# Kernel tuning notes

Hardware: AMD Instinct MI355X
Metric: run time of the kernel (lower is better)

## Reference

```python
import jax, jax.numpy as jnp
import numpy as np

B, T, DIM = 4, 1024, 2048
N_HEADS, N_KV_HEADS = 32, 8
HEAD_DIM = DIM // N_HEADS  # 64
N_REPS = N_HEADS // N_KV_HEADS  # 4


def setup_inputs() -> dict:
    key = jax.random.key(0)
    ks = jax.random.split(key, 8)
    # RoPE tables: theta = 10000^{-2i/d}, positions 0..T-1
    inv_freq = 1.0 / (10000.0 ** (jnp.arange(0, HEAD_DIM, 2, dtype=jnp.float32) / HEAD_DIM))
    angles = jnp.arange(T, dtype=jnp.float32)[:, None] * inv_freq[None, :]  # (T, HEAD_DIM//2)
    s = 0.02
    return {
        "input": jax.random.normal(ks[0], (B, T, DIM), jnp.float32),
        "freqs_cos": jnp.cos(angles),
        "freqs_sin": jnp.sin(angles),
        "mask": jnp.tril(jnp.ones((T, T), dtype=bool)),  # causal boolean mask
        "wq": s * jax.random.normal(ks[1], (DIM, DIM), jnp.float32),
        "wk": s * jax.random.normal(ks[2], (N_KV_HEADS * HEAD_DIM, DIM), jnp.float32),
        "wv": s * jax.random.normal(ks[3], (N_KV_HEADS * HEAD_DIM, DIM), jnp.float32),
        "wo": s * jax.random.normal(ks[4], (DIM, DIM), jnp.float32),
        "curr_pos": 0,
    }


def _apply_rope(x, cos, sin):
    # x: (B, T, H, D); cos/sin: (T, D//2). Complex multiply on (even, odd) pairs.
    xr = x[..., 0::2]
    xi = x[..., 1::2]
    c = cos[None, :, None, :]
    s = sin[None, :, None, :]
    out_r = xr * c - xi * s
    out_i = xr * s + xi * c
    return jnp.stack([out_r, out_i], axis=-1).reshape(x.shape)


def reference(input, freqs_cos, freqs_sin, mask, wq, wk, wv, wo, curr_pos):
    Bv, Tv = input.shape[0], input.shape[1]
    qs = (input @ wq.T).reshape(Bv, Tv, N_HEADS, HEAD_DIM)
    ks = (input @ wk.T).reshape(Bv, Tv, N_KV_HEADS, HEAD_DIM)
    vs = (input @ wv.T).reshape(Bv, Tv, N_KV_HEADS, HEAD_DIM)
    qs = _apply_rope(qs, freqs_cos, freqs_sin)
    ks = _apply_rope(ks, freqs_cos, freqs_sin)

    # KV cache (prefill path: curr_pos == 0, fresh cache of length 2T)
    kv_cache = jnp.zeros((Bv, 2 * Tv, N_KV_HEADS, HEAD_DIM, 2), input.dtype)
    kv_cache = kv_cache.at[:, curr_pos:curr_pos + Tv, :, :, 0].set(ks)
    kv_cache = kv_cache.at[:, curr_pos:curr_pos + Tv, :, :, 1].set(vs)
    k_all = kv_cache[:, :curr_pos + Tv, :, :, 0]
    v_all = kv_cache[:, :curr_pos + Tv, :, :, 1]

    # GQA: broadcast each kv head across its query-head group (avoid repeat_interleave copy)
    S = k_all.shape[1]
    q = qs.transpose(0, 2, 1, 3).reshape(Bv, N_KV_HEADS, N_REPS, Tv, HEAD_DIM)
    k = k_all.transpose(0, 2, 1, 3)  # (B, KVH, S, D)
    v = v_all.transpose(0, 2, 1, 3)

    scale = 1.0 / jnp.sqrt(jnp.asarray(HEAD_DIM, input.dtype))
    scores = jnp.einsum("bgrqd,bgkd->bgrqk", q, k) * scale  # (B, KVH, REPS, T, S)
    neg = jnp.asarray(jnp.finfo(input.dtype).min, input.dtype)
    scores = jnp.where(mask[None, None, None, :, :S], scores, neg)
    attn = jax.nn.softmax(scores, axis=-1)
    out = jnp.einsum("bgrqk,bgkd->bgrqd", attn, v)
    out = out.reshape(Bv, N_HEADS, Tv, HEAD_DIM).transpose(0, 2, 1, 3).reshape(Bv, Tv, DIM)
    return out @ wo.T
```

## Files before the change

### kernel.cpp

```cpp
#include <hip/hip_runtime.h>
#include <cstdint>

typedef __bf16 bf16x8 __attribute__((ext_vector_type(8)));
typedef float  f32x4  __attribute__((ext_vector_type(4)));
typedef float  f32x16 __attribute__((ext_vector_type(16)));
typedef float  float8v __attribute__((ext_vector_type(8)));
typedef unsigned short ushort8v __attribute__((ext_vector_type(8)));
typedef unsigned short ushort4v __attribute__((ext_vector_type(4)));
typedef unsigned int   uint4v   __attribute__((ext_vector_type(4)));

__device__ __forceinline__ unsigned short f2b(float f) {
  uint32_t u = __builtin_bit_cast(uint32_t, f);
  u += 0x7FFFu + ((u >> 16) & 1u);
  return (unsigned short)(u >> 16);
}
__device__ __forceinline__ float b2f(unsigned short h) {
  uint32_t u = ((uint32_t)h) << 16;
  return __builtin_bit_cast(float, u);
}
__device__ __forceinline__ unsigned int cvtpk(float lo, float hi_) {
  unsigned int r;
  asm("v_cvt_pk_bf16_f32 %0, %1, %2" : "=v"(r) : "v"(lo), "v"(hi_));
  return r;
}

__device__ __forceinline__ void async16(const void* g, void* l) {
  __builtin_amdgcn_global_load_lds(
      (const __attribute__((address_space(1))) void*)g,
      (__attribute__((address_space(3))) void*)l, 16, 0, 0);
}

#define WAITVM(N)  __builtin_amdgcn_s_waitcnt(0x0F70 | ((N) & 15))

struct CvtArgs {
  const float* src[5];
  unsigned short* dst[5];
  long n[5];
};
__global__ void cvt5_kernel(CvtArgs a) {
  long base = (long)blockIdx.x * blockDim.x + threadIdx.x;
  long gstride = (long)gridDim.x * blockDim.x;
#pragma unroll 1
  for (int sg = 0; sg < 5; ++sg) {
    const float* s = a.src[sg];
    unsigned short* d = a.dst[sg];
    long n8 = a.n[sg] >> 3;
    for (long i = base; i < n8; i += gstride) {
      float8v f = *(const float8v*)(s + i * 8);
      ushort8v o;
#pragma unroll
      for (int j = 0; j < 8; ++j) o[j] = f2b(f[j]);
      *(ushort8v*)(d + i * 8) = o;
    }
  }
}

__global__ __launch_bounds__(512, 2)
void gemmQ192(const unsigned short* __restrict__ Ag, const unsigned short* __restrict__ Wg,
              unsigned short* __restrict__ Cp) {
  constexpr int K = 2048;
  constexpr int NF = 3;
  constexpr int ASLOT = 16384;
  constexpr int BSLOT = 24576;
  constexpr int N = 3072;

  extern __shared__ char lds_c[];

  const int tid = threadIdx.x;
  const int wave = tid >> 6, lane = tid & 63;
  const int wm = wave >> 2, wn = wave & 3;
  const int lr = lane & 15, lg = lane >> 4;

  const int flat = blockIdx.y * 16 + blockIdx.x;
  const int swz = (flat & 7) * 32 + (flat >> 3);
  const int m0 = (swz >> 4) * 256, n0 = (swz & 15) * 192;

  const int laneSw = (lr >> 1) * 128 + (((((lr & 1) << 2) | lg) ^ (lr >> 1)) << 4);
  const int aoff = wm * 8192 + laneSw;

  int bByte[NF], bR7[NF];
#pragma unroll
  for (int ni = 0; ni < NF; ++ni) {
    int row = wn * 48 + ni * 16 + lr;
    bByte[ni] = row * 128;
    bR7[ni] = row & 7;
  }

  f32x4 acc[8][NF] = {};
  bf16x8 af[4], bf[NF];

  auto stA = [&](int slot, int s) {
    char* sl = lds_c + slot * ASLOT;
    const int kc = s * 32;
#pragma unroll
    for (int j = 0; j < 2; ++j) {
      int q = (tid + 512 * j) * 16;
      int R = q >> 7, g2L = ((q >> 4) & 7) ^ (R & 7);
      int row = R * 2 + (g2L >> 2), kg = g2L & 3;
      async16(Ag + (size_t)(m0 + row) * K + kc + kg * 8, sl + q);
    }
  };
  auto stB = [&](int slot, int T) {
    char* sl = lds_c + 4 * ASLOT + slot * BSLOT;
    const int kc = T * 64;
#pragma unroll
    for (int j = 0; j < 3; ++j) {
      int q = (tid + 512 * j) * 16;
      int row = q >> 7, c = (q >> 4) & 7;
      async16(Wg + (size_t)(n0 + row) * K + kc + ((c ^ (row & 7)) * 8), sl + q);
    }
  };

#define PH(SA, SB, MH, KH, RDB, STG, VM)                                      \
  {                                                                           \
    const char* As_ = lds_c + (SA) * ASLOT;                                   \
    _Pragma("unroll") for (int mi = 0; mi < 4; ++mi)                          \
      af[mi] = *(const bf16x8*)(As_ + aoff + ((MH) * 4 + mi) * 1024);         \
    if (RDB) {                                                                \
      const char* Bs_ = lds_c + 4 * ASLOT + (SB) * BSLOT;                     \
      _Pragma("unroll") for (int ni = 0; ni < NF; ++ni)                       \
        bf[ni] = *(const bf16x8*)(Bs_ + bByte[ni] +                           \
                                  (((((KH) << 2) | lg) ^ bR7[ni]) << 4));     \
    }                                                                         \
    STG;                                                                      \
    if ((VM) >= 0) WAITVM(VM);                                                \
    __builtin_amdgcn_s_barrier();                                             \
    __builtin_amdgcn_s_setprio(1);                                            \
    _Pragma("unroll") for (int mi = 0; mi < 4; ++mi)                          \
      _Pragma("unroll") for (int ni = 0; ni < NF; ++ni)                       \
        acc[(MH) * 4 + mi][ni] = __builtin_amdgcn_mfma_f32_16x16x32_bf16(     \
            af[mi], bf[ni], acc[(MH) * 4 + mi][ni], 0, 0, 0);                 \
    __builtin_amdgcn_s_setprio(0);                                            \
    __builtin_amdgcn_s_barrier();                                             \
  }

  stB(0, 0); stA(0, 0); stA(1, 1); stB(1, 1); stA(2, 2);
  WAITVM(5);
  __builtin_amdgcn_s_barrier();

  for (int t2 = 0; t2 < 30; t2 += 2) {
    PH(0, 0, 0, 0, true,  stA(3, 2 * t2 + 3), -1);
    PH(0, 0, 1, 0, false, (void)0, -1);
    PH(1, 0, 0, 1, true,  stA(0, 2 * t2 + 4), -1);
    PH(1, 0, 1, 1, false, stB(0, t2 + 2), 5);
    PH(2, 1, 0, 0, true,  stA(1, 2 * t2 + 5), -1);
    PH(2, 1, 1, 0, false, (void)0, -1);
    PH(3, 1, 0, 1, true,  stA(2, 2 * t2 + 6), -1);
    PH(3, 1, 1, 1, false, stB(1, t2 + 3), 5);
  }
  PH(0, 0, 0, 0, true,  stA(3, 63), -1);
  PH(0, 0, 1, 0, false, (void)0, -1);
  PH(1, 0, 0, 1, true,  (void)0, -1);
  PH(1, 0, 1, 1, false, (void)0, 0);
  PH(2, 1, 0, 0, true,  (void)0, -1);
  PH(2, 1, 1, 0, false, (void)0, -1);
  PH(3, 1, 0, 1, true,  (void)0, -1);
  PH(3, 1, 1, 1, false, (void)0, -1);
#undef PH

#pragma unroll
  for (int mig = 0; mig < 8; ++mig) {
#pragma unroll
    for (int j = 0; j < 4; ++j) {
      int row = m0 + wm * 128 + mig * 16 + lg * 4 + j;
#pragma unroll
      for (int ni = 0; ni < NF; ++ni) {
        int col = n0 + wn * 48 + ni * 16 + lr;
        Cp[(size_t)row * N + col] = f2b(acc[mig][ni][j]);
      }
    }
  }
}

template<bool F32OUT, int BN, int GX, int GY>
__global__ __launch_bounds__(512, 2)
void gemm8p(const unsigned short* __restrict__ Ag, const unsigned short* __restrict__ Wg,
            void* __restrict__ Cp, int N) {
  constexpr int K = 2048;
  constexpr int BM = 256;
  constexpr int NF = BN / 64;
  constexpr int AL = 2;
  constexpr int BL = BN / 128;
  constexpr int VMS = 2 * BL + AL;
  constexpr int ASLOT = BM * 64;
  constexpr int BSLOT = BN * 64;
  constexpr int NWG = GX * GY;
  constexpr int CPX = NWG / 8;

  extern __shared__ char lds_c[];

  const int tid = threadIdx.x;
  const int wave = tid >> 6, lane = tid & 63;
  const int wm = wave >> 2, wn = wave & 3;
  const int lr = lane & 15, lg = lane >> 4;

  const int flat = blockIdx.y * GX + blockIdx.x;
  const int swz = (flat & 7) * CPX + (flat >> 3);
  const int m0 = (swz / GX) * BM, n0 = (swz % GX) * BN;

  const int laneSw = (lr >> 1) * 128 + (((((lr & 1) << 2) | lg) ^ (lr >> 1)) << 4);
  const int aoff = wm * 128 * 64 + laneSw;
  const int boff = wn * NF * 1024 + laneSw;

  f32x4 acc[8][NF] = {};
  bf16x8 af[4], bf[NF];

  auto stA = [&](int slot, int s) {
    char* sl = lds_c + slot * ASLOT;
    const int kc = s * 32;
#pragma unroll
    for (int j = 0; j < AL; ++j) {
      int q = (tid + 512 * j) * 16;
      int R = q >> 7, g2L = ((q >> 4) & 7) ^ (R & 7);
      int row = R * 2 + (g2L >> 2), kg = g2L & 3;
      async16(Ag + (size_t)(m0 + row) * K + kc + kg * 8, sl + q);
    }
  };
  auto stB = [&](int slot, int s) {
    char* sl = lds_c + 4 * ASLOT + slot * BSLOT;
    const int kc = s * 32;
#pragma unroll
    for (int j = 0; j < BL; ++j) {
      int q = (tid + 512 * j) * 16;
      int R = q >> 7, g2L = ((q >> 4) & 7) ^ (R & 7);
      int row = R * 2 + (g2L >> 2), kg = g2L & 3;
      async16(Wg + (size_t)(n0 + row) * K + kc + kg * 8, sl + q);
    }
  };

#define PH(RSLOT, MH, RDB, STG, VM)                                           \
  {                                                                           \
    const char* As_ = lds_c + (RSLOT) * ASLOT;                                \
    _Pragma("unroll") for (int mi = 0; mi < 4; ++mi)                          \
      af[mi] = *(const bf16x8*)(As_ + aoff + ((MH) * 4 + mi) * 1024);         \
    if (RDB) {                                                                \
      const char* Bs_ = lds_c + 4 * ASLOT + (RSLOT) * BSLOT;                  \
      _Pragma("unroll") for (int ni = 0; ni < NF; ++ni)                       \
        bf[ni] = *(const bf16x8*)(Bs_ + boff + ni * 1024);                    \
    }                                                                         \
    STG;                                                                      \
    if ((VM) >= 0) WAITVM(VM);                                                \
    __builtin_amdgcn_s_barrier();                                             \
    __builtin_amdgcn_s_setprio(1);                                            \
    _Pragma("unroll") for (int mi = 0; mi < 4; ++mi)                          \
      _Pragma("unroll") for (int ni = 0; ni < NF; ++ni)                       \
        acc[(MH) * 4 + mi][ni] = __builtin_amdgcn_mfma_f32_16x16x32_bf16(     \
            af[mi], bf[ni], acc[(MH) * 4 + mi][ni], 0, 0, 0);                 \
    __builtin_amdgcn_s_setprio(0);                                            \
    __builtin_amdgcn_s_barrier();                                             \
  }

  stB(0, 0); stA(0, 0); stB(1, 1); stA(1, 1); stB(2, 2); stA(2, 2); stB(3, 3);
  WAITVM(VMS);
  __builtin_amdgcn_s_barrier();

  for (int T = 0; T < 30; T += 2) {
    const int p0 = 2 * T;
    PH(0, 0, true,  stA(3, p0 + 3), -1);
    PH(0, 1, false, stB(0, p0 + 4), -1);
    PH(1, 0, true,  stA(0, p0 + 4), -1);
    PH(1, 1, false, stB(1, p0 + 5), VMS);
    PH(2, 0, true,  stA(1, p0 + 5), -1);
    PH(2, 1, false, stB(2, p0 + 6), -1);
    PH(3, 0, true,  stA(2, p0 + 6), -1);
    PH(3, 1, false, stB(3, p0 + 7), VMS);
  }
  PH(0, 0, true,  stA(3, 63), -1);
  PH(0, 1, false, (void)0, -1);
  PH(1, 0, true,  (void)0, -1);
  PH(1, 1, false, (void)0, 0);
  PH(2, 0, true,  (void)0, -1);
  PH(2, 1, false, (void)0, -1);
  PH(3, 0, true,  (void)0, -1);
  PH(3, 1, false, (void)0, -1);
#undef PH

#pragma unroll
  for (int mig = 0; mig < 8; ++mig) {
#pragma unroll
    for (int j = 0; j < 4; ++j) {
      int row = m0 + wm * 128 + mig * 16 + lg * 4 + j;
#pragma unroll
      for (int ni = 0; ni < NF; ++ni) {
        int col = n0 + wn * (NF * 16) + ni * 16 + lr;
        float v = acc[mig][ni][j];
        if (F32OUT) ((float*)Cp)[(size_t)row * N + col] = v;
        else        ((unsigned short*)Cp)[(size_t)row * N + col] = f2b(v);
      }
    }
  }
}

__global__ __launch_bounds__(256)
void ropekv_kernel(unsigned short* __restrict__ qkv,
                   const float* __restrict__ cosb, const float* __restrict__ sinb,
                   unsigned short* __restrict__ vt) {
  const int tt0 = blockIdx.x * 64;
  const int kvh = blockIdx.y;
  const int b   = blockIdx.z;
  const int tid = threadIdx.x;

  {
    int r = tid >> 2, c0 = (tid & 3) * 16;
    int t = tt0 + r;
    unsigned short* kp = qkv + (size_t)(b * 1024 + t) * 3072 + 2048 + kvh * 64 + c0;
    const float* cb = cosb + t * 32 + c0 / 2;
    const float* sb = sinb + t * 32 + c0 / 2;
    ushort8v x0 = *(const ushort8v*)kp;
    ushort8v x1 = *(const ushort8v*)(kp + 8);
    float8v c = *(const float8v*)cb;
    float8v s = *(const float8v*)sb;
    ushort8v o0, o1;
#pragma unroll
    for (int j = 0; j < 4; ++j) {
      float xr = b2f(x0[2 * j]), xi = b2f(x0[2 * j + 1]);
      o0[2 * j]     = f2b(xr * c[j] - xi * s[j]);
      o0[2 * j + 1] = f2b(xr * s[j] + xi * c[j]);
    }
#pragma unroll
    for (int j = 0; j < 4; ++j) {
      float xr = b2f(x1[2 * j]), xi = b2f(x1[2 * j + 1]);
      o1[2 * j]     = f2b(xr * c[4 + j] - xi * s[4 + j]);
      o1[2 * j + 1] = f2b(xr * s[4 + j] + xi * c[4 + j]);
    }
    *(ushort8v*)kp = o0;
    *(ushort8v*)(kp + 8) = o1;
  }

  __shared__ unsigned short lT[64 * 68];
#pragma unroll
  for (int i = 0; i < 2; ++i) {
    int r = i * 32 + (tid >> 3), c = (tid & 7) * 8;
    const unsigned short* src = qkv + (size_t)(b * 1024 + tt0 + r) * 3072 + 2560 + kvh * 64 + c;
    ushort8v v = *(const ushort8v*)src;
    ushort4v a, b4;
#pragma unroll
    for (int j = 0; j < 4; ++j) { a[j] = v[j]; b4[j] = v[j + 4]; }
    *(ushort4v*)&lT[r * 68 + c]     = a;
    *(ushort4v*)&lT[r * 68 + c + 4] = b4;
  }
  __syncthreads();
#pragma unroll
  for (int i = 0; i < 2; ++i) {
    int d = tid & 63;
    int tt = i * 4 + (tid >> 6);
    ushort8v o;
#pragma unroll
    for (int j = 0; j < 8; ++j) o[j] = lT[(tt * 8 + j) * 68 + d];
    *(ushort8v*)&vt[((size_t)((b * 8 + kvh) * 64 + d)) * 1024 + tt0 + tt * 8] = o;
  }
}

__global__ __launch_bounds__(256, 2)
void attn_kernel(const unsigned short* __restrict__ qkv, const unsigned short* __restrict__ vt,
                 const float* __restrict__ cosb, const float* __restrict__ sinb,
                 unsigned short* __restrict__ ob) {
  const int flat = (blockIdx.z * 8 + blockIdx.y) * 16 + blockIdx.x;
  const int swzb = (flat & 7) * 64 + (flat >> 3);
  const int bx = swzb & 15, kvh = (swzb >> 4) & 7, b = swzb >> 7;

  const int tid = threadIdx.x, wave = tid >> 6, lane = tid & 63;
  const int l31 = lane & 31, hi = lane >> 5;
  const int h = kvh * 4 + wave;

  const int qth = 31 - bx, qtl = bx;
  const int q0h = qth * 32, q0l = qtl * 32;
  const int nth = qth / 4 + 1, ntl = qtl / 4 + 1;
  const int ntot = nth + ntl;

  __shared__ unsigned short lK[2][128 * 64];
  __shared__ unsigned short lVt[2][64 * 128];

  auto ldq = [&](int q0, bf16x8* qf) {
    int t = q0 + l31;
    const unsigned short* qp = qkv + (size_t)(b * 1024 + t) * 3072 + h * 64;
#pragma unroll
    for (int dk = 0; dk < 4; ++dk) {
      ushort8v q = *(const ushort8v*)(qp + dk * 16 + hi * 8);
      f32x4 c4 = *(const f32x4*)(cosb + t * 32 + dk * 8 + hi * 4);
      f32x4 s4 = *(const f32x4*)(sinb + t * 32 + dk * 8 + hi * 4);
      ushort8v o;
#pragma unroll
      for (int j = 0; j < 4; ++j) {
        float xr = b2f(q[2 * j]), xi = b2f(q[2 * j + 1]);
        o[2 * j]     = f2b(xr * c4[j] - xi * s4[j]);
        o[2 * j + 1] = f2b(xr * s4[j] + xi * c4[j]);
      }
      qf[dk] = __builtin_bit_cast(bf16x8, o);
    }
  };

  const unsigned short* kg = qkv + (size_t)(b * 1024) * 3072 + 2048 + kvh * 64;
  const unsigned short* vg = vt + (size_t)(b * 8 + kvh) * 64 * 1024;

  auto stage = [&](int kvb, int bi) {
    const int sr  = tid >> 3;
    const int scb = (tid & 7) * 16;
#pragma unroll
    for (int i = 0; i < 4; ++i) {
      int r = i * 32 + sr;
      int cb = scb ^ ((r & 7) << 4);
      async16(kg + (size_t)(kvb + r) * 3072 + (cb >> 1), &lK[bi][r * 64 + (scb >> 1)]);
    }
    const int rv0 = tid >> 4;
    const int scv = (tid & 15) * 16;
#pragma unroll
    for (int i = 0; i < 4; ++i) {
      int rv = i * 16 + rv0;
      int cbv = scv ^ ((rv & 15) << 4);
      async16(vg + (size_t)rv * 1024 + kvb + (cbv >> 1), &lVt[bi][rv * 128 + (scv >> 1)]);
    }
  };

  bf16x8 qf[4];
  f32x16 oacc[2] = {};
  float m2 = -3e38f, l_run = 0.f;
  int q0 = q0h;

  ldq(q0h, qf);

  const float SC = 0.125f * 1.44269504f;

  auto chunk64 = [&](int cur, int ckvb, int c, bool lastT) {
    f32x16 sd[2] = {};
    __builtin_amdgcn_s_setprio(1);
#pragma unroll
    for (int s = 0; s < 2; ++s) {
      const int krow = c * 64 + s * 32 + l31;
      const char* kr = (const char*)lK[cur] + krow * 128;
      const int swz = (krow & 7) << 4;
#pragma unroll
      for (int dk = 0; dk < 4; ++dk) {
        bf16x8 kf = *(const bf16x8*)(kr + ((dk * 32 + hi * 16) ^ swz));
        sd[s] = __builtin_amdgcn_mfma_f32_32x32x16_bf16(kf, qf[dk], sd[s], 0, 0, 0);
      }
    }
    __builtin_amdgcn_s_setprio(0);

#pragma unroll
    for (int s = 0; s < 2; ++s)
#pragma unroll
      for (int r = 0; r < 16; ++r) {
        float v = sd[s][r] * SC;
        if (lastT) {
          int kvg = ckvb + s * 32 + (r & 3) + 8 * (r >> 2) + 4 * hi;
          if (kvg > q0 + l31) v = -3e38f;
        }
        sd[s][r] = v;
      }
    float pm = sd[0][0];
#pragma unroll
    for (int s = 0; s < 2; ++s)
#pragma unroll
      for (int r = 0; r < 16; ++r) pm = fmaxf(pm, sd[s][r]);
    pm = fmaxf(pm, __shfl_xor(pm, 32));
    if (!__all(pm <= m2 + 11.0f)) {
      float mnew = fmaxf(m2, pm);
      float alpha = exp2f(m2 - mnew);
      m2 = mnew;
      l_run *= alpha;
#pragma unroll
      for (int db = 0; db < 2; ++db)
#pragma unroll
        for (int r = 0; r < 16; ++r) oacc[db][r] *= alpha;
    }
    float tsum = 0.f;
#pragma unroll
    for (int s = 0; s < 2; ++s)
#pragma unroll
      for (int r = 0; r < 16; ++r) { float p = exp2f(sd[s][r] - m2); sd[s][r] = p; tsum += p; }
    tsum += __shfl_xor(tsum, 32);
    l_run += tsum;

    bf16x8 pf[2][2];
#pragma unroll
    for (int s = 0; s < 2; ++s)
#pragma unroll
      for (int kc = 0; kc < 2; ++kc) {
        unsigned int cA = cvtpk(sd[s][8 * kc + 0], sd[s][8 * kc + 1]);
        unsigned int cB = cvtpk(sd[s][8 * kc + 4], sd[s][8 * kc + 5]);
        unsigned int cC = cvtpk(sd[s][8 * kc + 2], sd[s][8 * kc + 3]);
        unsigned int cD = cvtpk(sd[s][8 * kc + 6], sd[s][8 * kc + 7]);
        unsigned int xA = __shfl_xor(cA, 32), xB = __shfl_xor(cB, 32);
        unsigned int xC = __shfl_xor(cC, 32), xD = __shfl_xor(cD, 32);
        uint4v u;
        u[0] = hi ? xB : cA;
        u[1] = hi ? xD : cC;
        u[2] = hi ? cB : xA;
        u[3] = hi ? cD : xC;
        pf[s][kc] = __builtin_bit_cast(bf16x8, u);
      }

    __builtin_amdgcn_s_setprio(1);
#pragma unroll
    for (int db = 0; db < 2; ++db) {
      const int row = db * 32 + l31;
      const char* vr = (const char*)lVt[cur] + row * 256;
      const int vswz = (row & 15) << 4;
#pragma unroll
      for (int s = 0; s < 2; ++s)
#pragma unroll
        for (int kc = 0; kc < 2; ++kc) {
          bf16x8 vf = *(const bf16x8*)(vr + ((c * 128 + s * 64 + kc * 32 + hi * 16) ^ vswz));
          oacc[db] = __builtin_amdgcn_mfma_f32_32x32x16_bf16(vf, pf[s][kc], oacc[db], 0, 0, 0);
        }
    }
    __builtin_amdgcn_s_setprio(0);
  };

  auto writeOut = [&](int q0w) {
    float inv = 1.0f / l_run;
    unsigned short* orow = ob + (size_t)(b * 1024 + q0w + l31) * 2048 + h * 64;
#pragma unroll
    for (int db = 0; db < 2; ++db)
#pragma unroll
      for (int g = 0; g < 4; ++g) {
        int d0 = db * 32 + 8 * g + 4 * hi;
        ushort4v o;
#pragma unroll
        for (int j = 0; j < 4; ++j) o[j] = f2b(oacc[db][4 * g + j] * inv);
        *(ushort4v*)(orow + d0) = o;
      }
  };

  auto kvb_of = [&](int j) { return (j < nth ? j : j - nth) * 128; };

  stage(0, 0);
  __syncthreads();

  for (int j = 0; j < ntot; ++j) {
    const int cur = j & 1;
    if (j + 1 < ntot) stage(kvb_of(j + 1), cur ^ 1);
    const int kvb = kvb_of(j);
    const bool lastT = (j == nth - 1) || (j == ntot - 1);

#pragma unroll 1
    for (int c = 0; c < 2; ++c) {
      if (kvb + c * 64 > q0 + 31) continue;
      chunk64(cur, kvb + c * 64, c, lastT);
    }

    if (j == nth - 1) {
      writeOut(q0h);
      oacc[0] = f32x16{}; oacc[1] = f32x16{};
      m2 = -3e38f; l_run = 0.f;
      q0 = q0l;
      ldq(q0l, qf);
    }
    __syncthreads();
  }
  writeOut(q0l);
}

extern "C" void kernel_launch(void* const* d_in, const int* in_sizes, int n_in,
                              void* d_out, int out_size, void* d_ws, size_t ws_size,
                              hipStream_t stream) {
  const float* input = (const float*)d_in[0];
  const float* fcos  = (const float*)d_in[1];
  const float* fsin  = (const float*)d_in[2];
  const float* wq = (const float*)d_in[4];
  const float* wk = (const float*)d_in[5];
  const float* wv = (const float*)d_in[6];
  const float* wo = (const float*)d_in[7];
  float* out = (float*)d_out;

  unsigned short* xb   = (unsigned short*)d_ws;
  unsigned short* wqkv = xb + (size_t)4096 * 2048;
  unsigned short* wob  = wqkv + (size_t)3072 * 2048;
  unsigned short* qkv  = wob + (size_t)2048 * 2048;
  unsigned short* ob   = qkv + (size_t)4096 * 3072;
  unsigned short* vtb  = xb;

  hipFuncSetAttribute((const void*)&gemmQ192,
                      hipFuncAttributeMaxDynamicSharedMemorySize, 114688);
  hipFuncSetAttribute((const void*)&gemm8p<true, 128, 16, 16>,
                      hipFuncAttributeMaxDynamicSharedMemorySize, 98304);

  CvtArgs ca;
  ca.src[0] = input; ca.dst[0] = xb;                        ca.n[0] = (long)4096 * 2048;
  ca.src[1] = wq;    ca.dst[1] = wqkv;                      ca.n[1] = (long)2048 * 2048;
  ca.src[2] = wk;    ca.dst[2] = wqkv + (size_t)2048 * 2048; ca.n[2] = (long)512 * 2048;
  ca.src[3] = wv;    ca.dst[3] = wqkv + (size_t)2560 * 2048; ca.n[3] = (long)512 * 2048;
  ca.src[4] = wo;    ca.dst[4] = wob;                       ca.n[4] = (long)2048 * 2048;
  hipLaunchKernelGGL(cvt5_kernel, dim3(2048), dim3(256), 0, stream, ca);

  hipLaunchKernelGGL(gemmQ192, dim3(16, 16), dim3(512), 114688,
                     stream, xb, wqkv, qkv);

  hipLaunchKernelGGL(ropekv_kernel, dim3(16, 8, 4), dim3(256), 0, stream,
                     qkv, fcos, fsin, vtb);

  hipLaunchKernelGGL(attn_kernel, dim3(16, 8, 4), dim3(256), 0, stream,
                     qkv, vtb, fcos, fsin, ob);

  hipLaunchKernelGGL((gemm8p<true, 128, 16, 16>), dim3(16, 16), dim3(512), 98304,
                     stream, ob, wob, (void*)out, 2048);
}
```

Baseline: 163.9 us.

## Process paired causal q-tiles concurrently with 8 waves sharing K/V stages

Doubles the attention block to 512 threads so that waves 0-3 handle the high (long) query tile and waves 4-7 handle the low (short) tile at the same time. Both groups reuse the same staged K/V chunks, so the low tile's K/V tiles are no longer loaded a second time, and each thread issues half as many async copies. Waves on the short tile sit idle at barriers once they finish, which could leave the combined work unevenly spread. Launch bounds change to (512,4), which limits registers per thread.

After: 163.5 us. No clear change (-0.2%).

```diff
diff --git a/kernel.cpp b/kernel.cpp
--- a/kernel.cpp
+++ b/kernel.cpp
@@ -351,7 +351,7 @@
   }
 }
 
-__global__ __launch_bounds__(256, 2)
+__global__ __launch_bounds__(512, 4)
 void attn_kernel(const unsigned short* __restrict__ qkv, const unsigned short* __restrict__ vt,
                  const float* __restrict__ cosb, const float* __restrict__ sinb,
                  unsigned short* __restrict__ ob) {
@@ -361,17 +361,19 @@
 
   const int tid = threadIdx.x, wave = tid >> 6, lane = tid & 63;
   const int l31 = lane & 31, hi = lane >> 5;
-  const int h = kvh * 4 + wave;
+  const int wq = wave & 3, wh = wave >> 2;
+  const int h = kvh * 4 + wq;
 
   const int qth = 31 - bx, qtl = bx;
-  const int q0h = qth * 32, q0l = qtl * 32;
   const int nth = qth / 4 + 1, ntl = qtl / 4 + 1;
-  const int ntot = nth + ntl;
+  const int q0 = (wh ? qtl : qth) * 32;
+  const int nt = wh ? ntl : nth;
 
   __shared__ unsigned short lK[2][128 * 64];
   __shared__ unsigned short lVt[2][64 * 128];
 
-  auto ldq = [&](int q0, bf16x8* qf) {
+  bf16x8 qf[4];
+  {
     int t = q0 + l31;
     const unsigned short* qp = qkv + (size_t)(b * 1024 + t) * 3072 + h * 64;
 #pragma unroll
@@ -388,7 +390,7 @@
       }
       qf[dk] = __builtin_bit_cast(bf16x8, o);
     }
-  };
+  }
 
   const unsigned short* kg = qkv + (size_t)(b * 1024) * 3072 + 2048 + kvh * 64;
   const unsigned short* vg = vt + (size_t)(b * 8 + kvh) * 64 * 1024;
@@ -397,27 +399,23 @@
     const int sr  = tid >> 3;
     const int scb = (tid & 7) * 16;
 #pragma unroll
-    for (int i = 0; i < 4; ++i) {
-      int r = i * 32 + sr;
+    for (int i = 0; i < 2; ++i) {
+      int r = i * 64 + sr;
       int cb = scb ^ ((r & 7) << 4);
       async16(kg + (size_t)(kvb + r) * 3072 + (cb >> 1), &lK[bi][r * 64 + (scb >> 1)]);
     }
     const int rv0 = tid >> 4;
     const int scv = (tid & 15) * 16;
 #pragma unroll
-    for (int i = 0; i < 4; ++i) {
-      int rv = i * 16 + rv0;
+    for (int i = 0; i < 2; ++i) {
+      int rv = i * 32 + rv0;
       int cbv = scv ^ ((rv & 15) << 4);
       async16(vg + (size_t)rv * 1024 + kvb + (cbv >> 1), &lVt[bi][rv * 128 + (scv >> 1)]);
     }
   };
 
-  bf16x8 qf[4];
   f32x16 oacc[2] = {};
   float m2 = -3e38f, l_run = 0.f;
-  int q0 = q0h;
-
-  ldq(q0h, qf);
 
   const float SC = 0.125f * 1.44269504f;
 
@@ -508,9 +506,28 @@
     __builtin_amdgcn_s_setprio(0);
   };
 
-  auto writeOut = [&](int q0w) {
+  stage(0, 0);
+  __syncthreads();
+
+  for (int j = 0; j < nth; ++j) {
+    const int cur = j & 1;
+    if (j + 1 < nth) stage((j + 1) * 128, cur ^ 1);
+    const int kvb = j * 128;
+
+    if (j < nt) {
+      const bool lastT = (j == nt - 1);
+#pragma unroll 1
+      for (int c = 0; c < 2; ++c) {
+        if (kvb + c * 64 > q0 + 31) continue;
+        chunk64(cur, kvb + c * 64, c, lastT);
+      }
+    }
+    __syncthreads();
+  }
+
+  {
     float inv = 1.0f / l_run;
-    unsigned short* orow = ob + (size_t)(b * 1024 + q0w + l31) * 2048 + h * 64;
+    unsigned short* orow = ob + (size_t)(b * 1024 + q0 + l31) * 2048 + h * 64;
 #pragma unroll
     for (int db = 0; db < 2; ++db)
 #pragma unroll
@@ -521,35 +538,7 @@
         for (int j = 0; j < 4; ++j) o[j] = f2b(oacc[db][4 * g + j] * inv);
         *(ushort4v*)(orow + d0) = o;
       }
-  };
-
-  auto kvb_of = [&](int j) { return (j < nth ? j : j - nth) * 128; };
-
-  stage(0, 0);
-  __syncthreads();
-
-  for (int j = 0; j < ntot; ++j) {
-    const int cur = j & 1;
-    if (j + 1 < ntot) stage(kvb_of(j + 1), cur ^ 1);
-    const int kvb = kvb_of(j);
-    const bool lastT = (j == nth - 1) || (j == ntot - 1);
-
-#pragma unroll 1
-    for (int c = 0; c < 2; ++c) {
-      if (kvb + c * 64 > q0 + 31) continue;
-      chunk64(cur, kvb + c * 64, c, lastT);
-    }
-
-    if (j == nth - 1) {
-      writeOut(q0h);
-      oacc[0] = f32x16{}; oacc[1] = f32x16{};
-      m2 = -3e38f; l_run = 0.f;
-      q0 = q0l;
-      ldq(q0l, qf);
-    }
-    __syncthreads();
-  }
-  writeOut(q0l);
+  }
 }
 
 extern "C" void kernel_launch(void* const* d_in, const int* in_sizes, int n_in,
@@ -590,7 +579,7 @@
   hipLaunchKernelGGL(ropekv_kernel, dim3(16, 8, 4), dim3(256), 0, stream,
                      qkv, fcos, fsin, vtb);
 
-  hipLaunchKernelGGL(attn_kernel, dim3(16, 8, 4), dim3(256), 0, stream,
+  hipLaunchKernelGGL(attn_kernel, dim3(16, 8, 4), dim3(512), 0, stream,
                      qkv, vtb, fcos, fsin, ob);
 
   hipLaunchKernelGGL((gemm8p<true, 128, 16, 16>), dim3(16, 16), dim3(512), 98304,
```
